# Kernel optimization log

Hardware: AMD Instinct MI355X
Metric: run time of the kernel (lower is better)

The kernel has to match this reference:

```python
import jax, jax.numpy as jnp
import numpy as np

B = 4096
D = 256
TEMP = 0.5


def setup_inputs() -> dict:
    key = jax.random.key(0)
    k1, k2 = jax.random.split(key)
    x_i = jax.random.normal(k1, (B, D), dtype=jnp.float32)
    x_j = jax.random.normal(k2, (B, D), dtype=jnp.float32)
    return {"x_i": x_i, "x_j": x_j}


def reference(x_i, x_j):
    b = x_i.shape[0]
    # L2-normalize rows (F.normalize with default eps=1e-12)
    def l2norm(x):
        n = jnp.linalg.norm(x, axis=1, keepdims=True)
        return x / jnp.maximum(n, 1e-12)

    z = jnp.concatenate([l2norm(x_i), l2norm(x_j)], axis=0)  # [2B, D]
    # rows of z are unit-norm, so cosine similarity == dot product
    sim = z @ z.T  # [2B, 2B]

    # positives: diagonals at offsets +B and -B
    idx = jnp.arange(b)
    sim_ij = sim[idx, idx + b]
    sim_ji = sim[idx + b, idx]
    pos = jnp.concatenate([sim_ij, sim_ji], axis=0)  # [2B]

    nom = jnp.exp(pos / TEMP)
    neg_mask = 1.0 - jnp.eye(2 * b, dtype=sim.dtype)
    denom = jnp.sum(neg_mask * jnp.exp(sim / TEMP), axis=1)  # [2B]
    loss = jnp.sum(-jnp.log(nom / denom)) / (2 * b)
    return loss
```

## Files before the change

### kernel.cpp

```cpp
#include <hip/hip_runtime.h>

#define NB   4096
#define ND   256
#define N2B  8192
#define INV_T 2.0f

typedef __attribute__((ext_vector_type(8))) short bf16x8;
typedef __attribute__((ext_vector_type(4))) float f32x4;

__device__ __forceinline__ void gload_lds16(const void* g, void* l) {
  __builtin_amdgcn_global_load_lds(
      (const __attribute__((address_space(1))) void*)g,
      (__attribute__((address_space(3))) void*)l, 16, 0, 0);
}

__device__ __forceinline__ unsigned short f2b(float f) {
  unsigned int u = __float_as_uint(f);
  u = (u + 0x7fffu + ((u >> 16) & 1u)) >> 16;
  return (unsigned short)u;
}
__device__ __forceinline__ float b2f(unsigned short h) {
  return __uint_as_float(((unsigned int)h) << 16);
}

__global__ __launch_bounds__(256) void k_normalize(
    const float* __restrict__ xi, const float* __restrict__ xj,
    unsigned short* __restrict__ Z, float* __restrict__ diagE,
    float* __restrict__ pos, float* __restrict__ lossAcc,
    unsigned int* __restrict__ ticket) {
  __shared__ float sh[2][256];
  if (blockIdx.x == 0 && threadIdx.x == 0) { *lossAcc = 0.0f; *ticket = 0u; }
  int wave = threadIdx.x >> 6, lane = threadIdx.x & 63;
  int r = (int)blockIdx.x * 2 + (wave & 1);
  bool isJ = wave >= 2;
  const float* src = (isJ ? xj : xi) + (size_t)r * ND;
  int zrow = r + (isJ ? NB : 0);

  float4 v = *(const float4*)(src + lane * 4);
  float ss = v.x * v.x + v.y * v.y + v.z * v.z + v.w * v.w;
#pragma unroll
  for (int m = 1; m < 64; m <<= 1) ss += __shfl_xor(ss, m, 64);
  float scale = 1.0f / fmaxf(sqrtf(ss), 1e-12f);
  unsigned short h0 = f2b(v.x * scale), h1 = f2b(v.y * scale);
  unsigned short h2 = f2b(v.z * scale), h3 = f2b(v.w * scale);
  ushort4 st; st.x = h0; st.y = h1; st.z = h2; st.w = h3;
  *(ushort4*)(Z + (size_t)zrow * ND + lane * 4) = st;

  float f0 = b2f(h0), f1 = b2f(h1), f2 = b2f(h2), f3 = b2f(h3);
  float d = f0 * f0 + f1 * f1 + f2 * f2 + f3 * f3;
#pragma unroll
  for (int m = 1; m < 64; m <<= 1) d += __shfl_xor(d, m, 64);
  if (lane == 0) diagE[zrow] = __expf(d * INV_T);

  if (isJ) {
    float* s = sh[wave & 1] + lane * 4;
    s[0] = f0; s[1] = f1; s[2] = f2; s[3] = f3;
  }
  __syncthreads();
  if (!isJ) {
    const float* s = sh[wave] + lane * 4;
    float p = f0 * s[0] + f1 * s[1] + f2 * s[2] + f3 * s[3];
#pragma unroll
    for (int m = 1; m < 64; m <<= 1) p += __shfl_xor(p, m, 64);
    if (lane == 0) pos[r] = p;
  }
}

#define CT 64
__global__ __launch_bounds__(256) void k_gemm_exp(
    const unsigned short* __restrict__ Z, float* __restrict__ R) {
  __shared__ alignas(16) unsigned short Bs[CT * ND];

  int tid = threadIdx.x;
  int wave = tid >> 6, lane = tid & 63;
  int band = (int)blockIdx.x >> 3;
  int colq = (int)blockIdx.x & 7;
  int quad = lane >> 4, c16 = lane & 15;

  bf16x8 afr[2][8];
  int rowA = band * 128 + wave * 32;
#pragma unroll
  for (int rg = 0; rg < 2; ++rg)
#pragma unroll
    for (int kk = 0; kk < 8; ++kk)
      afr[rg][kk] = *(const bf16x8*)(Z + (size_t)(rowA + rg * 16 + c16) * ND +
                                     kk * 32 + quad * 8);

  float rs[2][4];
#pragma unroll
  for (int rg = 0; rg < 2; ++rg)
#pragma unroll
    for (int r = 0; r < 4; ++r) rs[rg][r] = 0.0f;

  int lr1 = lane >> 5;
  int cs = lane & 31;

  for (int ct = 0; ct < 16; ++ct) {
    int colbase = colq * 1024 + ct * CT;
    __syncthreads();
#pragma unroll
    for (int j = 0; j < 8; ++j) {
      int r0 = wave * 16 + j * 2;
      int row = r0 + lr1;
      int gc = cs ^ (row & 31);
      gload_lds16(Z + (size_t)(colbase + row) * ND + gc * 8, &Bs[r0 * ND]);
    }
    asm volatile("s_waitcnt vmcnt(0)" ::: "memory");
    __syncthreads();

    f32x4 acc[2][4] = {};
#pragma unroll
    for (int kk = 0; kk < 8; ++kk) {
      bf16x8 bfr[4];
#pragma unroll
      for (int ni = 0; ni < 4; ++ni) {
        int row = ni * 16 + c16;
        int slot = (kk * 4 + quad) ^ (row & 31);
        bfr[ni] = *(const bf16x8*)&Bs[row * ND + slot * 8];
      }
#pragma unroll
      for (int rg = 0; rg < 2; ++rg)
#pragma unroll
        for (int ni = 0; ni < 4; ++ni)
          acc[rg][ni] = __builtin_amdgcn_mfma_f32_16x16x32_bf16(
              afr[rg][kk], bfr[ni], acc[rg][ni], 0, 0, 0);
    }

#pragma unroll
    for (int rg = 0; rg < 2; ++rg)
#pragma unroll
      for (int ni = 0; ni < 4; ++ni)
#pragma unroll
        for (int r = 0; r < 4; ++r)
          rs[rg][r] += __expf(acc[rg][ni][r] * INV_T);
  }

#pragma unroll
  for (int m = 1; m <= 8; m <<= 1)
#pragma unroll
    for (int rg = 0; rg < 2; ++rg)
#pragma unroll
      for (int r = 0; r < 4; ++r)
        rs[rg][r] += __shfl_xor(rs[rg][r], m, 64);

#pragma unroll
  for (int rg = 0; rg < 2; ++rg)
#pragma unroll
    for (int r = 0; r < 4; ++r)
      if (c16 == rg * 4 + r) {
        int row = rowA + rg * 16 + quad * 4 + r;
        R[(size_t)row * 8 + colq] = rs[rg][r];
      }
}

__global__ __launch_bounds__(256) void k_final(
    const float* __restrict__ R, const float* __restrict__ diagE,
    const float* __restrict__ pos, float* __restrict__ lossAcc,
    unsigned int* __restrict__ ticket, float* __restrict__ out) {
  __shared__ float red[4];
  int tid = threadIdx.x;
  int wave = tid >> 6, lane = tid & 63;
  int row = (int)blockIdx.x * 256 + tid;

  const float* Rr = R + (size_t)row * 8;
  float4 a = *(const float4*)(Rr);
  float4 b = *(const float4*)(Rr + 4);
  float s = (a.x + a.y + a.z + a.w) + (b.x + b.y + b.z + b.w) - diagE[row];
  float term = __logf(s) - INV_T * pos[row & (NB - 1)];
#pragma unroll
  for (int m = 1; m < 64; m <<= 1) term += __shfl_xor(term, m, 64);
  if (lane == 0) red[wave] = term;
  __syncthreads();
  if (tid == 0) {
    float bs = red[0] + red[1] + red[2] + red[3];
    atomicAdd(lossAcc, bs);
    __threadfence();
    unsigned int old = atomicAdd(ticket, 1u);
    if (old == 31u) {
      float v = atomicAdd(lossAcc, 0.0f);
      out[0] = v * (1.0f / (float)N2B);
    }
  }
}

extern "C" void kernel_launch(void* const* d_in, const int* in_sizes, int n_in,
                              void* d_out, int out_size, void* d_ws,
                              size_t ws_size, hipStream_t stream) {
  const float* xi = (const float*)d_in[0];
  const float* xj = (const float*)d_in[1];
  float* out = (float*)d_out;
  char* ws = (char*)d_ws;
  unsigned short* Z = (unsigned short*)ws;
  float* R = (float*)(ws + (4u << 20));
  float* pos = (float*)(ws + (8u << 20));
  float* diagE = (float*)(ws + (8u << 20) + 65536);
  float* lossAcc = (float*)(ws + (8u << 20) + 131072);
  unsigned int* ticket = (unsigned int*)(ws + (8u << 20) + 131072 + 64);

  k_normalize<<<dim3(NB / 2), dim3(256), 0, stream>>>(xi, xj, Z, diagE, pos,
                                                      lossAcc, ticket);
  k_gemm_exp<<<dim3(512), dim3(256), 0, stream>>>(Z, R);
  k_final<<<dim3(32), dim3(256), 0, stream>>>(R, diagE, pos, lossAcc, ticket,
                                              out);
}
```

Before: 100.3 us.

## Exploit symmetry of similarity matrix with upper-triangular tile GEMM

Replaces the full 8192x8192 GEMM+exp with a kernel that computes only upper-triangular 128x128 tiles (2080 blocks), producing both row sums and, for off-diagonal tiles, column sums that stand in for the mirrored tile. Partial sums are written to a per-row 64-slot buffer that the final kernel reduces. This roughly halves the MFMA and exp work, at the cost of extra column reductions through LDS, a larger partial-sum buffer, and a triangular index mapping. It also sets launch bounds for two blocks per CU and raises wave priority during the MFMA loop.

```diff
diff --git a/kernel.cpp b/kernel.cpp
--- a/kernel.cpp
+++ b/kernel.cpp
@@ -4,6 +4,8 @@
 #define ND   256
 #define N2B  8192
 #define INV_T 2.0f
+#define NBAND 64
+#define NTRI  2080
 
 typedef __attribute__((ext_vector_type(8))) short bf16x8;
 typedef __attribute__((ext_vector_type(4))) float f32x4;
@@ -66,74 +68,84 @@
   }
 }
 
-#define CT 64
-__global__ __launch_bounds__(256) void k_gemm_exp(
-    const unsigned short* __restrict__ Z, float* __restrict__ R) {
-  __shared__ alignas(16) unsigned short Bs[CT * ND];
+__global__ __launch_bounds__(256, 2) void k_sym(
+    const unsigned short* __restrict__ Z, float* __restrict__ P) {
+  __shared__ alignas(16) unsigned short Bs[128 * ND];
 
   int tid = threadIdx.x;
   int wave = tid >> 6, lane = tid & 63;
-  int band = (int)blockIdx.x >> 3;
-  int colq = (int)blockIdx.x & 7;
   int quad = lane >> 4, c16 = lane & 15;
 
+  int t = (int)blockIdx.x;
+  t = (t & 7) * (NTRI / 8) + (t >> 3);
+  int I = (int)((129.0f - sqrtf(16641.0f - 8.0f * (float)t)) * 0.5f);
+  while (64 * (I + 1) - ((I + 1) * I) / 2 <= t) ++I;
+  while (64 * I - (I * (I - 1)) / 2 > t) --I;
+  int J = I + (t - (64 * I - (I * (I - 1)) / 2));
+  bool diag = (I == J);
+
+  int rowA = I * 128, rowB = J * 128;
+
+  int lr1 = lane >> 5, cs = lane & 31;
+#pragma unroll
+  for (int j = 0; j < 16; ++j) {
+    int r0 = wave * 32 + j * 2;
+    int row = r0 + lr1;
+    int gc = cs ^ (row & 31);
+    gload_lds16(Z + (size_t)(rowB + row) * ND + gc * 8, &Bs[r0 * ND]);
+  }
+
   bf16x8 afr[2][8];
-  int rowA = band * 128 + wave * 32;
+  int wrow = rowA + wave * 32;
 #pragma unroll
   for (int rg = 0; rg < 2; ++rg)
 #pragma unroll
     for (int kk = 0; kk < 8; ++kk)
-      afr[rg][kk] = *(const bf16x8*)(Z + (size_t)(rowA + rg * 16 + c16) * ND +
+      afr[rg][kk] = *(const bf16x8*)(Z + (size_t)(wrow + rg * 16 + c16) * ND +
                                      kk * 32 + quad * 8);
 
+  asm volatile("s_waitcnt vmcnt(0)" ::: "memory");
+  __syncthreads();
+
+  f32x4 acc[2][8] = {};
+  __builtin_amdgcn_s_setprio(1);
+#pragma unroll
+  for (int kk = 0; kk < 8; ++kk) {
+    bf16x8 bfr[8];
+#pragma unroll
+    for (int ni = 0; ni < 8; ++ni) {
+      int row = ni * 16 + c16;
+      int slot = (kk * 4 + quad) ^ (row & 31);
+      bfr[ni] = *(const bf16x8*)&Bs[row * ND + slot * 8];
+    }
+#pragma unroll
+    for (int rg = 0; rg < 2; ++rg)
+#pragma unroll
+      for (int ni = 0; ni < 8; ++ni)
+        acc[rg][ni] = __builtin_amdgcn_mfma_f32_16x16x32_bf16(
+            afr[rg][kk], bfr[ni], acc[rg][ni], 0, 0, 0);
+  }
+  __builtin_amdgcn_s_setprio(0);
+
   float rs[2][4];
+  float csum[8];
+#pragma unroll
+  for (int ni = 0; ni < 8; ++ni) csum[ni] = 0.0f;
 #pragma unroll
   for (int rg = 0; rg < 2; ++rg)
 #pragma unroll
     for (int r = 0; r < 4; ++r) rs[rg][r] = 0.0f;
 
-  int lr1 = lane >> 5;
-  int cs = lane & 31;
-
-  for (int ct = 0; ct < 16; ++ct) {
-    int colbase = colq * 1024 + ct * CT;
-    __syncthreads();
-#pragma unroll
-    for (int j = 0; j < 8; ++j) {
-      int r0 = wave * 16 + j * 2;
-      int row = r0 + lr1;
-      int gc = cs ^ (row & 31);
-      gload_lds16(Z + (size_t)(colbase + row) * ND + gc * 8, &Bs[r0 * ND]);
-    }
-    asm volatile("s_waitcnt vmcnt(0)" ::: "memory");
-    __syncthreads();
-
-    f32x4 acc[2][4] = {};
-#pragma unroll
-    for (int kk = 0; kk < 8; ++kk) {
-      bf16x8 bfr[4];
-#pragma unroll
-      for (int ni = 0; ni < 4; ++ni) {
-        int row = ni * 16 + c16;
-        int slot = (kk * 4 + quad) ^ (row & 31);
-        bfr[ni] = *(const bf16x8*)&Bs[row * ND + slot * 8];
+#pragma unroll
+  for (int rg = 0; rg < 2; ++rg)
+#pragma unroll
+    for (int ni = 0; ni < 8; ++ni)
+#pragma unroll
+      for (int r = 0; r < 4; ++r) {
+        float e = __expf(acc[rg][ni][r] * INV_T);
+        rs[rg][r] += e;
+        csum[ni] += e;
       }
-#pragma unroll
-      for (int rg = 0; rg < 2; ++rg)
-#pragma unroll
-        for (int ni = 0; ni < 4; ++ni)
-          acc[rg][ni] = __builtin_amdgcn_mfma_f32_16x16x32_bf16(
-              afr[rg][kk], bfr[ni], acc[rg][ni], 0, 0, 0);
-    }
-
-#pragma unroll
-    for (int rg = 0; rg < 2; ++rg)
-#pragma unroll
-      for (int ni = 0; ni < 4; ++ni)
-#pragma unroll
-        for (int r = 0; r < 4; ++r)
-          rs[rg][r] += __expf(acc[rg][ni][r] * INV_T);
-  }
 
 #pragma unroll
   for (int m = 1; m <= 8; m <<= 1)
@@ -148,13 +160,34 @@
 #pragma unroll
     for (int r = 0; r < 4; ++r)
       if (c16 == rg * 4 + r) {
-        int row = rowA + rg * 16 + quad * 4 + r;
-        R[(size_t)row * 8 + colq] = rs[rg][r];
+        int row = wrow + rg * 16 + quad * 4 + r;
+        P[(size_t)row * NBAND + J] = rs[rg][r];
       }
+
+  if (!diag) {
+#pragma unroll
+    for (int ni = 0; ni < 8; ++ni) {
+      csum[ni] += __shfl_xor(csum[ni], 16, 64);
+      csum[ni] += __shfl_xor(csum[ni], 32, 64);
+    }
+    __syncthreads();
+    float* colred = (float*)Bs;
+    if (lane < 16) {
+#pragma unroll
+      for (int ni = 0; ni < 8; ++ni)
+        colred[wave * 128 + ni * 16 + lane] = csum[ni];
+    }
+    __syncthreads();
+    if (tid < 128) {
+      float v = colred[tid] + colred[128 + tid] + colred[256 + tid] +
+                colred[384 + tid];
+      P[(size_t)(rowB + tid) * NBAND + I] = v;
+    }
+  }
 }
 
 __global__ __launch_bounds__(256) void k_final(
-    const float* __restrict__ R, const float* __restrict__ diagE,
+    const float* __restrict__ P, const float* __restrict__ diagE,
     const float* __restrict__ pos, float* __restrict__ lossAcc,
     unsigned int* __restrict__ ticket, float* __restrict__ out) {
   __shared__ float red[4];
@@ -162,10 +195,14 @@
   int wave = tid >> 6, lane = tid & 63;
   int row = (int)blockIdx.x * 256 + tid;
 
-  const float* Rr = R + (size_t)row * 8;
-  float4 a = *(const float4*)(Rr);
-  float4 b = *(const float4*)(Rr + 4);
-  float s = (a.x + a.y + a.z + a.w) + (b.x + b.y + b.z + b.w) - diagE[row];
+  const float4* Pr = (const float4*)(P + (size_t)row * NBAND);
+  float s = 0.0f;
+#pragma unroll
+  for (int q = 0; q < 16; ++q) {
+    float4 a = Pr[q];
+    s += (a.x + a.y) + (a.z + a.w);
+  }
+  s -= diagE[row];
   float term = __logf(s) - INV_T * pos[row & (NB - 1)];
 #pragma unroll
   for (int m = 1; m < 64; m <<= 1) term += __shfl_xor(term, m, 64);
@@ -191,15 +228,15 @@
   float* out = (float*)d_out;
   char* ws = (char*)d_ws;
   unsigned short* Z = (unsigned short*)ws;
-  float* R = (float*)(ws + (4u << 20));
-  float* pos = (float*)(ws + (8u << 20));
-  float* diagE = (float*)(ws + (8u << 20) + 65536);
-  float* lossAcc = (float*)(ws + (8u << 20) + 131072);
-  unsigned int* ticket = (unsigned int*)(ws + (8u << 20) + 131072 + 64);
+  float* P = (float*)(ws + (4u << 20));
+  float* pos = (float*)(ws + (6u << 20));
+  float* diagE = (float*)(ws + (6u << 20) + 65536);
+  float* lossAcc = (float*)(ws + (6u << 20) + 131072);
+  unsigned int* ticket = (unsigned int*)(ws + (6u << 20) + 131072 + 64);
 
   k_normalize<<<dim3(NB / 2), dim3(256), 0, stream>>>(xi, xj, Z, diagE, pos,
                                                       lossAcc, ticket);
-  k_gemm_exp<<<dim3(512), dim3(256), 0, stream>>>(Z, R);
-  k_final<<<dim3(32), dim3(256), 0, stream>>>(R, diagE, pos, lossAcc, ticket,
+  k_sym<<<dim3(NTRI), dim3(256), 0, stream>>>(Z, P);
+  k_final<<<dim3(32), dim3(256), 0, stream>>>(P, diagE, pos, lossAcc, ticket,
                                               out);
 }
```

Measured after the change: 105.2 us. +4.8%, slower.
